# Kernel tuning notes

Measured on AMD Instinct MI355X. Metric: run time of the kernel, lower is better.

The kernel has to match this reference:

```python
import jax, jax.numpy as jnp
import numpy as np

NUM_HEADS = 16
NUM_KV_HEADS = 4
HEAD_SIZE = 128
SCALE = 1.0 / np.sqrt(128.0).astype(np.float32)
NEG_INF = -1e30


def setup_inputs() -> dict:
    key = jax.random.key(0)
    kq, kk, kv = jax.random.split(key, 3)
    B, S = 2, 2048
    query = jax.random.normal(kq, (B, NUM_HEADS, S, HEAD_SIZE), dtype=jnp.float32)
    k = jax.random.normal(kk, (B, NUM_KV_HEADS, S, HEAD_SIZE), dtype=jnp.float32)
    v = jax.random.normal(kv, (B, NUM_KV_HEADS, S, HEAD_SIZE), dtype=jnp.float32)
    return {"query": query, "key": k, "value": v}


def _attn(query, key, value):
    # query: [B, H, S, D]; key/value: [B, Hkv, S, D]; GQA with group = H // Hkv
    B, H, S, D = query.shape
    Hkv = key.shape[1]
    G = H // Hkv
    q = query.reshape(B, Hkv, G, S, D)
    # scores: [B, Hkv, G, Sq, Sk]
    scores = jnp.einsum('bkgsd,bktd->bkgst', q, key) * jnp.float32(SCALE)
    causal = jnp.tril(jnp.ones((S, S), dtype=bool))  # [Sq, Sk]
    scores = jnp.where(causal, scores, jnp.float32(NEG_INF))
    probs = jax.nn.softmax(scores, axis=-1)
    out = jnp.einsum('bkgst,bktd->bkgsd', probs, value)  # [B, Hkv, G, S, D]
    out = out.reshape(B, H, S, D)
    # transpose(1,2).reshape -> [B, S, H*D]
    return out.transpose(0, 2, 1, 3).reshape(B, S, H * D)


def reference(query, key, value):
    return _attn(query, key, value)
```

## Files before the change

kernel.cpp:

```cpp
#include <hip/hip_runtime.h>


#define S_LEN 2048
#define DH    128
#define NH    16
#define NKVH  4
#define NB    2
#define TQ    128
#define TK    64
#define NQT   (S_LEN / TQ)
#define QSCALE 0.12752749610559243f

typedef __attribute__((ext_vector_type(8))) short short8;
typedef __attribute__((ext_vector_type(4))) float f32x4;

#if __has_builtin(__builtin_amdgcn_exp2f)
#define EX2(x) __builtin_amdgcn_exp2f(x)
#else
#define EX2(x) exp2f(x)
#endif

__device__ __forceinline__ unsigned pk2(float a, float b) {
    union { float f; unsigned u; } x, y; x.f = a; y.f = b;
    return ((x.u + 0x8000u) >> 16) | ((y.u + 0x8000u) & 0xffff0000u);
}
__device__ __forceinline__ void cp16(const void* g, void* lds) {
    __builtin_amdgcn_global_load_lds(
        (const __attribute__((address_space(1))) void*)g,
        (__attribute__((address_space(3))) void*)lds, 16, 0, 0);
}

__global__ __launch_bounds__(256, 4)
void prepack(const float* __restrict__ K, const float* __restrict__ V,
             unsigned short* __restrict__ Kb, unsigned short* __restrict__ Vt) {
    if (blockIdx.y == 0) {
        const long long flat = (long long)blockIdx.x * 2048 + threadIdx.x * 8;
        const int s = (int)(flat >> 7) & (S_LEN - 1);
        const int d0 = (int)flat & 127;
        const float* p = K + flat;
        float4 x = *(const float4*)p;
        float4 y = *(const float4*)(p + 4);
        const int cs = (d0 >> 3) ^ (s & 7);
        uint4 o;
        o.x = pk2(x.x, x.y); o.y = pk2(x.z, x.w);
        o.z = pk2(y.x, y.y); o.w = pk2(y.z, y.w);
        *(uint4*)(Kb + (flat & ~127LL) + cs * 8) = o;
    } else {
        const int x = blockIdx.x;
        const int bkvh = x >> 7, sblk = (x >> 2) & 31, q = x & 3;
        const int tid = threadIdx.x;
        __shared__ unsigned Lt[64][17];
        const float* base = V + (size_t)bkvh * S_LEN * DH + (size_t)sblk * 64 * DH + q * 32;
#pragma unroll
        for (int j = 0; j < 2; ++j) {
            const int e = tid + j * 256;
            const int s = e >> 3, c4 = e & 7;
            float4 v = *(const float4*)(base + (size_t)s * DH + c4 * 4);
            Lt[s][c4 * 2]     = pk2(v.x, v.y);
            Lt[s][c4 * 2 + 1] = pk2(v.z, v.w);
        }
        __syncthreads();
        const unsigned short* lt = (const unsigned short*)&Lt[0][0];
        const int d_loc = tid >> 3, pc = tid & 7;
        const int d = q * 32 + d_loc;
        const int c_log = pc ^ (d & 7);
        unsigned short vv[8];
#pragma unroll
        for (int j = 0; j < 8; ++j) {
            const int kp = c_log * 8 + j;
            const int kv = ((kp >> 5) & 1) * 32 + ((kp >> 2) & 1) * 16
                         + ((kp >> 3) & 3) * 4 + (kp & 3);
            vv[j] = lt[kv * 34 + d_loc];
        }
        uint4 o;
        o.x = (unsigned)vv[0] | ((unsigned)vv[1] << 16);
        o.y = (unsigned)vv[2] | ((unsigned)vv[3] << 16);
        o.z = (unsigned)vv[4] | ((unsigned)vv[5] << 16);
        o.w = (unsigned)vv[6] | ((unsigned)vv[7] << 16);
        *(uint4*)(Vt + (size_t)bkvh * S_LEN * DH + (size_t)d * S_LEN + sblk * 64 + pc * 8) = o;
    }
}

__global__ __launch_bounds__(512, 4)
void attn_fwd(const float* __restrict__ Q,
              const unsigned short* __restrict__ Kb,
              const unsigned short* __restrict__ Vtg,
              float* __restrict__ O,
              float* __restrict__ Opart,
              float* __restrict__ Lpart) {
    const int n    = blockIdx.x;
    const int g    = n & 7;
    const int b    = g >> 2;
    const int kvh  = g & 3;
    const int kk   = n >> 3;
    const int h    = kvh * 4 + (kk & 3);
    const int pr   = kk >> 2;
    const int a    = pr & 7;
    const int role = pr >> 3;
    const int sid  = ((b * NH + h) << 3) + a;

    const int tid  = threadIdx.x;
    const int w    = tid >> 6;
    const int lane = tid & 63;
    const int quad = lane >> 4;
    const int l16  = lane & 15;
    const int swz  = l16 & 7;

    int qt0, kt00, nr0, qt1; bool two_seg;
    if (role == 0) { qt0 = a;      kt00 = 0;         nr0 = 2 * a + 2;
                     qt1 = 15 - a; two_seg = true; }
    else           { qt0 = 15 - a; kt00 = 15 - 2*a;  nr0 = 17;
                     qt1 = 0;      two_seg = false; }

    __shared__ alignas(16) unsigned short Kl[2][TK][DH];
    __shared__ alignas(16) unsigned short Vl[2][DH][TK];

    const unsigned short* kb = Kb  + ((size_t)b * NKVH + kvh) * (size_t)(S_LEN * DH);
    const unsigned short* vb = Vtg + ((size_t)b * NKVH + kvh) * (size_t)(S_LEN * DH);

    auto stage = [&](int buf, int kt) {
        const char* ks = (const char*)(kb + (size_t)kt * TK * DH);
        char* kd = (char*)&Kl[buf][0][0];
#pragma unroll
        for (int i = 0; i < 2; ++i) {
            const int off = w * 2048 + i * 1024;
            cp16(ks + off + lane * 16, kd + off);
        }
        const char* vs = (const char*)vb + (size_t)kt * (TK * 2);
        char* vd = (char*)&Vl[buf][0][0];
#pragma unroll
        for (int i = 0; i < 2; ++i) {
            const int off = w * 2048 + i * 1024;
            const int row = w * 16 + i * 8 + (lane >> 3);
            cp16(vs + (size_t)row * (S_LEN * 2) + (lane & 7) * 16, vd + off);
        }
    };
    auto ktof = [&](int r) { return r < nr0 ? kt00 + r : r - nr0; };

    stage(0, ktof(0));

    int qt  = qt0;
    int wq0 = qt * TQ + w * 16;
    int ntw = 2 * qt + 1 + (w >> 2);

    short8 aq[4];
    auto loadQ = [&]() {
        const float* qp = Q + (((size_t)b * NH + h) * S_LEN + wq0 + l16) * DH;
#pragma unroll
        for (int dc = 0; dc < 4; ++dc) {
            float4 xx = *(const float4*)(qp + dc * 32 + quad * 8);
            float4 yy = *(const float4*)(qp + dc * 32 + quad * 8 + 4);
            union { unsigned u[4]; short8 s; } tq;
            tq.u[0] = pk2(xx.x * QSCALE, xx.y * QSCALE);
            tq.u[1] = pk2(xx.z * QSCALE, xx.w * QSCALE);
            tq.u[2] = pk2(yy.x * QSCALE, yy.y * QSCALE);
            tq.u[3] = pk2(yy.z * QSCALE, yy.w * QSCALE);
            aq[dc] = tq.s;
        }
    };
    loadQ();

    f32x4 o[8];
    float lsum = 0.f;
#pragma unroll
    for (int ch = 0; ch < 8; ++ch) o[ch] = (f32x4){0.f, 0.f, 0.f, 0.f};

    __syncthreads();

    int cur = 0;
    for (int r = 0; r < 17; ++r) {
        if (r + 1 < 17) stage(cur ^ 1, ktof(r + 1));
        const int kt = ktof(r);
        if (kt < ntw) {
            const int j0 = kt * TK;
            const bool diag = (kt == ntw - 1);
            f32x4 s[4];
#pragma unroll
            for (int k4 = 0; k4 < 4; ++k4) s[k4] = (f32x4){0.f, 0.f, 0.f, 0.f};
#pragma unroll
            for (int dc = 0; dc < 4; ++dc) {
#pragma unroll
                for (int k4 = 0; k4 < 4; ++k4) {
                    short8 bk = *(const short8*)&Kl[cur][k4 * 16 + l16][((dc * 4 + quad) ^ swz) * 8];
                    s[k4] = __builtin_amdgcn_mfma_f32_16x16x32_bf16(bk, aq[dc], s[k4], 0, 0, 0);
                }
            }
            const int qrow = wq0 + l16;
            float p[4][4];
#pragma unroll
            for (int k4 = 0; k4 < 4; ++k4) {
#pragma unroll
                for (int rr = 0; rr < 4; ++rr) {
                    float v = s[k4][rr];
                    if (diag && (j0 + k4 * 16 + quad * 4 + rr > qrow)) v = -1e30f;
                    const float pe = EX2(v);
                    lsum += pe;
                    p[k4][rr] = pe;
                }
            }
            union { unsigned u[4]; short8 s8; } pa0, pa1;
            pa0.u[0] = pk2(p[0][0], p[0][1]); pa0.u[1] = pk2(p[0][2], p[0][3]);
            pa0.u[2] = pk2(p[1][0], p[1][1]); pa0.u[3] = pk2(p[1][2], p[1][3]);
            pa1.u[0] = pk2(p[2][0], p[2][1]); pa1.u[1] = pk2(p[2][2], p[2][3]);
            pa1.u[2] = pk2(p[3][0], p[3][1]); pa1.u[3] = pk2(p[3][2], p[3][3]);
#pragma unroll
            for (int ch = 0; ch < 8; ++ch) {
                short8 bv0 = *(const short8*)&Vl[cur][ch * 16 + l16][(quad ^ swz) * 8];
                o[ch] = __builtin_amdgcn_mfma_f32_16x16x32_bf16(pa0.s8, bv0, o[ch], 0, 0, 0);
                short8 bv1 = *(const short8*)&Vl[cur][ch * 16 + l16][((4 + quad) ^ swz) * 8];
                o[ch] = __builtin_amdgcn_mfma_f32_16x16x32_bf16(pa1.s8, bv1, o[ch], 0, 0, 0);
            }
        }
        __syncthreads();
        cur ^= 1;
        if (two_seg && r == nr0 - 1) {
            float rs = lsum;
            rs += __shfl_xor(rs, 16);
            rs += __shfl_xor(rs, 32);
#pragma unroll
            for (int rr = 0; rr < 4; ++rr) {
                const float invl = 1.f / __shfl(rs, quad * 4 + rr);
                const int row = wq0 + quad * 4 + rr;
                float* op = O + ((size_t)b * S_LEN + row) * (NH * DH) + h * DH;
#pragma unroll
                for (int ch = 0; ch < 8; ++ch)
                    op[ch * 16 + l16] = o[ch][rr] * invl;
            }
            qt = qt1; wq0 = qt * TQ + w * 16; ntw = 2 * qt + 1 + (w >> 2);
            loadQ();
#pragma unroll
            for (int ch = 0; ch < 8; ++ch) o[ch] = (f32x4){0.f, 0.f, 0.f, 0.f};
            lsum = 0.f;
        }
    }

    float* lb = Lpart + (size_t)(role * 256 + sid) * 128;
    {
        float rs = lsum;
        rs += __shfl_xor(rs, 16);
        rs += __shfl_xor(rs, 32);
        if (lane < 16) lb[w * 16 + l16] = rs;
#pragma unroll
        for (int rr = 0; rr < 4; ++rr) {
            const int rl = w * 16 + quad * 4 + rr;
            float* op;
            if (role == 0) {
                const int row = wq0 + quad * 4 + rr;
                op = O + ((size_t)b * S_LEN + row) * (NH * DH) + h * DH;
            } else {
                op = Opart + (size_t)sid * (128 * 128) + (size_t)rl * 128;
            }
#pragma unroll
            for (int ch = 0; ch < 8; ++ch)
                op[ch * 16 + l16] = o[ch][rr];
        }
    }
}

__global__ __launch_bounds__(256)
void combine(const float* __restrict__ Opart, const float* __restrict__ Lpart,
             float* __restrict__ O) {
    const int blk = blockIdx.x;
    const int sid = blk >> 2;
    const int qp  = blk & 3;
    const int bh = sid >> 3, a = sid & 7;
    const int b = bh >> 4, h = bh & 15;
    const int qt = 15 - a;
    const float* o1 = Opart + (size_t)sid * (128 * 128);
    const float* l0 = Lpart + (size_t)sid * 128;
    const float* l1 = Lpart + (size_t)(256 + sid) * 128;
    const int tid = threadIdx.x;
#pragma unroll
    for (int i = 0; i < 4; ++i) {
        const int idx = qp * 1024 + i * 256 + tid;
        const int row = idx >> 5;
        const int c4  = idx & 31;
        const float inv = 1.f / (l0[row] + l1[row]);
        float* op = O + ((size_t)b * S_LEN + qt * 128 + row) * (NH * DH) + h * DH + c4 * 4;
        const float4 x = *(const float4*)op;
        const float4 y = ((const float4*)o1)[idx];
        float4 z;
        z.x = (x.x + y.x) * inv; z.y = (x.y + y.y) * inv;
        z.z = (x.z + y.z) * inv; z.w = (x.w + y.w) * inv;
        *(float4*)op = z;
    }
}

extern "C" void kernel_launch(void* const* d_in, const int* in_sizes, int n_in,
                              void* d_out, int out_size, void* d_ws, size_t ws_size,
                              hipStream_t stream) {
    const float* Q = (const float*)d_in[0];
    const float* K = (const float*)d_in[1];
    const float* V = (const float*)d_in[2];
    float* O = (float*)d_out;
    unsigned short* Kb = (unsigned short*)d_ws;
    unsigned short* Vt = Kb + (size_t)NB * NKVH * S_LEN * DH;
    float* Opart = (float*)(Vt + (size_t)NB * NKVH * S_LEN * DH);
    float* Lpart = Opart + (size_t)256 * 128 * 128;
    dim3 pgrid(NB * NKVH * (S_LEN / 16), 2);
    prepack<<<pgrid, 256, 0, stream>>>(K, V, Kb, Vt);
    attn_fwd<<<dim3(512), 512, 0, stream>>>(Q, Kb, Vt, O, Opart, Lpart);
    combine<<<dim3(1024), 256, 0, stream>>>(Opart, Lpart, O);
}
```

Baseline: 146.6 us.

## Split KV tile across wave pairs with 32-row query tiles and LDS reduction

Each wave now owns 32 query rows, two 16-row sub-tiles, and half of the 64-key tile. Each K and V fragment read from LDS is reused across two MFMAs, which halves LDS traffic per MFMA. Partial outputs and row sums from paired waves are summed through shared memory, reusing the idle K/V double-buffer slots plus a new 16KB exchange buffer, before the normalize or store step. The cost is more registers for two accumulator sets, extra LDS capacity that may lower occupancy, and several added barriers at segment boundaries.

```diff
diff --git a/kernel.cpp b/kernel.cpp
--- a/kernel.cpp
+++ b/kernel.cpp
@@ -101,6 +101,8 @@
 
     const int tid  = threadIdx.x;
     const int w    = tid >> 6;
+    const int rw   = w >> 1;
+    const int kh   = w & 1;
     const int lane = tid & 63;
     const int quad = lane >> 4;
     const int l16  = lane & 15;
@@ -114,6 +116,7 @@
 
     __shared__ alignas(16) unsigned short Kl[2][TK][DH];
     __shared__ alignas(16) unsigned short Vl[2][DH][TK];
+    __shared__ alignas(16) float XCH[4096];
 
     const unsigned short* kb = Kb  + ((size_t)b * NKVH + kvh) * (size_t)(S_LEN * DH);
     const unsigned short* vb = Vtg + ((size_t)b * NKVH + kvh) * (size_t)(S_LEN * DH);
@@ -139,120 +142,207 @@
 
     stage(0, ktof(0));
 
-    int qt  = qt0;
-    int wq0 = qt * TQ + w * 16;
-    int ntw = 2 * qt + 1 + (w >> 2);
-
-    short8 aq[4];
+    int qt, wq0, ntw;
+    auto setseg = [&](int q) {
+        qt = q; wq0 = qt * TQ + rw * 32;
+        ntw = (wq0 + 31 - kh * 32 + 64) >> 6;
+    };
+    setseg(qt0);
+
+    short8 aq[2][4];
     auto loadQ = [&]() {
-        const float* qp = Q + (((size_t)b * NH + h) * S_LEN + wq0 + l16) * DH;
-#pragma unroll
-        for (int dc = 0; dc < 4; ++dc) {
-            float4 xx = *(const float4*)(qp + dc * 32 + quad * 8);
-            float4 yy = *(const float4*)(qp + dc * 32 + quad * 8 + 4);
-            union { unsigned u[4]; short8 s; } tq;
-            tq.u[0] = pk2(xx.x * QSCALE, xx.y * QSCALE);
-            tq.u[1] = pk2(xx.z * QSCALE, xx.w * QSCALE);
-            tq.u[2] = pk2(yy.x * QSCALE, yy.y * QSCALE);
-            tq.u[3] = pk2(yy.z * QSCALE, yy.w * QSCALE);
-            aq[dc] = tq.s;
+#pragma unroll
+        for (int sub = 0; sub < 2; ++sub) {
+            const float* qp = Q + (((size_t)b * NH + h) * S_LEN + wq0 + sub * 16 + l16) * DH;
+#pragma unroll
+            for (int dc = 0; dc < 4; ++dc) {
+                float4 xx = *(const float4*)(qp + dc * 32 + quad * 8);
+                float4 yy = *(const float4*)(qp + dc * 32 + quad * 8 + 4);
+                union { unsigned u[4]; short8 s; } tq;
+                tq.u[0] = pk2(xx.x * QSCALE, xx.y * QSCALE);
+                tq.u[1] = pk2(xx.z * QSCALE, xx.w * QSCALE);
+                tq.u[2] = pk2(yy.x * QSCALE, yy.y * QSCALE);
+                tq.u[3] = pk2(yy.z * QSCALE, yy.w * QSCALE);
+                aq[sub][dc] = tq.s;
+            }
         }
     };
     loadQ();
 
-    f32x4 o[8];
-    float lsum = 0.f;
-#pragma unroll
-    for (int ch = 0; ch < 8; ++ch) o[ch] = (f32x4){0.f, 0.f, 0.f, 0.f};
+    f32x4 o[2][8];
+    float lsum[2] = {0.f, 0.f};
+#pragma unroll
+    for (int sub = 0; sub < 2; ++sub)
+#pragma unroll
+        for (int ch = 0; ch < 8; ++ch) o[sub][ch] = (f32x4){0.f, 0.f, 0.f, 0.f};
+
+    int cur = 0;
+
+    auto pair_reduce = [&](float rs[2]) {
+        f32x4* dA = (f32x4*)&XCH[0];
+        f32x4* dB = (f32x4*)&Kl[cur ^ 1][0][0];
+        f32x4* dC = (f32x4*)&Vl[cur ^ 1][0][0];
+        float* rsb = (float*)&Kl[cur ^ 1][0][0];
+        if (w == 1 || w == 3 || w == 5) {
+            f32x4* d = (w == 1) ? dA : (w == 3) ? dB : dC;
+#pragma unroll
+            for (int sub = 0; sub < 2; ++sub)
+#pragma unroll
+                for (int ch = 0; ch < 8; ++ch)
+                    d[(sub * 8 + ch) * 64 + lane] = o[sub][ch];
+        }
+        __syncthreads();
+        if (w == 0 || w == 2 || w == 4) {
+            f32x4* d = (w == 0) ? dA : (w == 2) ? dB : dC;
+#pragma unroll
+            for (int sub = 0; sub < 2; ++sub)
+#pragma unroll
+                for (int ch = 0; ch < 8; ++ch)
+                    o[sub][ch] += d[(sub * 8 + ch) * 64 + lane];
+        }
+        __syncthreads();
+        if (w == 7) {
+#pragma unroll
+            for (int sub = 0; sub < 2; ++sub)
+#pragma unroll
+                for (int ch = 0; ch < 8; ++ch)
+                    dA[(sub * 8 + ch) * 64 + lane] = o[sub][ch];
+        }
+        if ((w & 1) && lane < 16) {
+            rsb[rw * 32 + l16]      = rs[0];
+            rsb[rw * 32 + 16 + l16] = rs[1];
+        }
+        __syncthreads();
+        if (w == 6) {
+#pragma unroll
+            for (int sub = 0; sub < 2; ++sub)
+#pragma unroll
+                for (int ch = 0; ch < 8; ++ch)
+                    o[sub][ch] += dA[(sub * 8 + ch) * 64 + lane];
+        }
+        if (!(w & 1)) {
+            rs[0] += rsb[rw * 32 + l16];
+            rs[1] += rsb[rw * 32 + 16 + l16];
+        }
+        __syncthreads();
+    };
+    auto rowsum = [&](float rs[2]) {
+#pragma unroll
+        for (int sub = 0; sub < 2; ++sub) {
+            float t = lsum[sub];
+            t += __shfl_xor(t, 16);
+            t += __shfl_xor(t, 32);
+            rs[sub] = t;
+        }
+    };
 
     __syncthreads();
 
-    int cur = 0;
     for (int r = 0; r < 17; ++r) {
         if (r + 1 < 17) stage(cur ^ 1, ktof(r + 1));
         const int kt = ktof(r);
         if (kt < ntw) {
             const int j0 = kt * TK;
             const bool diag = (kt == ntw - 1);
-            f32x4 s[4];
-#pragma unroll
-            for (int k4 = 0; k4 < 4; ++k4) s[k4] = (f32x4){0.f, 0.f, 0.f, 0.f};
+            f32x4 s[2][2];
+#pragma unroll
+            for (int sub = 0; sub < 2; ++sub)
+#pragma unroll
+                for (int k2 = 0; k2 < 2; ++k2) s[sub][k2] = (f32x4){0.f, 0.f, 0.f, 0.f};
 #pragma unroll
             for (int dc = 0; dc < 4; ++dc) {
 #pragma unroll
-                for (int k4 = 0; k4 < 4; ++k4) {
-                    short8 bk = *(const short8*)&Kl[cur][k4 * 16 + l16][((dc * 4 + quad) ^ swz) * 8];
-                    s[k4] = __builtin_amdgcn_mfma_f32_16x16x32_bf16(bk, aq[dc], s[k4], 0, 0, 0);
+                for (int k2 = 0; k2 < 2; ++k2) {
+                    short8 bk = *(const short8*)&Kl[cur][kh * 32 + k2 * 16 + l16][((dc * 4 + quad) ^ swz) * 8];
+                    s[0][k2] = __builtin_amdgcn_mfma_f32_16x16x32_bf16(bk, aq[0][dc], s[0][k2], 0, 0, 0);
+                    s[1][k2] = __builtin_amdgcn_mfma_f32_16x16x32_bf16(bk, aq[1][dc], s[1][k2], 0, 0, 0);
                 }
             }
-            const int qrow = wq0 + l16;
-            float p[4][4];
-#pragma unroll
-            for (int k4 = 0; k4 < 4; ++k4) {
-#pragma unroll
-                for (int rr = 0; rr < 4; ++rr) {
-                    float v = s[k4][rr];
-                    if (diag && (j0 + k4 * 16 + quad * 4 + rr > qrow)) v = -1e30f;
-                    const float pe = EX2(v);
-                    lsum += pe;
-                    p[k4][rr] = pe;
+            union { unsigned u[4]; short8 s8; } pa[2];
+#pragma unroll
+            for (int sub = 0; sub < 2; ++sub) {
+                const int qrow = wq0 + sub * 16 + l16;
+                float p[2][4];
+#pragma unroll
+                for (int k2 = 0; k2 < 2; ++k2) {
+#pragma unroll
+                    for (int rr = 0; rr < 4; ++rr) {
+                        float v = s[sub][k2][rr];
+                        if (diag && (j0 + kh * 32 + k2 * 16 + quad * 4 + rr > qrow)) v = -1e30f;
+                        const float pe = EX2(v);
+                        lsum[sub] += pe;
+                        p[k2][rr] = pe;
+                    }
                 }
-            }
-            union { unsigned u[4]; short8 s8; } pa0, pa1;
-            pa0.u[0] = pk2(p[0][0], p[0][1]); pa0.u[1] = pk2(p[0][2], p[0][3]);
-            pa0.u[2] = pk2(p[1][0], p[1][1]); pa0.u[3] = pk2(p[1][2], p[1][3]);
-            pa1.u[0] = pk2(p[2][0], p[2][1]); pa1.u[1] = pk2(p[2][2], p[2][3]);
-            pa1.u[2] = pk2(p[3][0], p[3][1]); pa1.u[3] = pk2(p[3][2], p[3][3]);
+                pa[sub].u[0] = pk2(p[0][0], p[0][1]);
+                pa[sub].u[1] = pk2(p[0][2], p[0][3]);
+                pa[sub].u[2] = pk2(p[1][0], p[1][1]);
+                pa[sub].u[3] = pk2(p[1][2], p[1][3]);
+            }
 #pragma unroll
             for (int ch = 0; ch < 8; ++ch) {
-                short8 bv0 = *(const short8*)&Vl[cur][ch * 16 + l16][(quad ^ swz) * 8];
-                o[ch] = __builtin_amdgcn_mfma_f32_16x16x32_bf16(pa0.s8, bv0, o[ch], 0, 0, 0);
-                short8 bv1 = *(const short8*)&Vl[cur][ch * 16 + l16][((4 + quad) ^ swz) * 8];
-                o[ch] = __builtin_amdgcn_mfma_f32_16x16x32_bf16(pa1.s8, bv1, o[ch], 0, 0, 0);
+                short8 bv = *(const short8*)&Vl[cur][ch * 16 + l16][((kh * 4 + quad) ^ swz) * 8];
+                o[0][ch] = __builtin_amdgcn_mfma_f32_16x16x32_bf16(pa[0].s8, bv, o[0][ch], 0, 0, 0);
+                o[1][ch] = __builtin_amdgcn_mfma_f32_16x16x32_bf16(pa[1].s8, bv, o[1][ch], 0, 0, 0);
             }
         }
         __syncthreads();
         cur ^= 1;
         if (two_seg && r == nr0 - 1) {
-            float rs = lsum;
-            rs += __shfl_xor(rs, 16);
-            rs += __shfl_xor(rs, 32);
-#pragma unroll
-            for (int rr = 0; rr < 4; ++rr) {
-                const float invl = 1.f / __shfl(rs, quad * 4 + rr);
-                const int row = wq0 + quad * 4 + rr;
-                float* op = O + ((size_t)b * S_LEN + row) * (NH * DH) + h * DH;
-#pragma unroll
-                for (int ch = 0; ch < 8; ++ch)
-                    op[ch * 16 + l16] = o[ch][rr] * invl;
-            }
-            qt = qt1; wq0 = qt * TQ + w * 16; ntw = 2 * qt + 1 + (w >> 2);
+            float rs[2];
+            rowsum(rs);
+            pair_reduce(rs);
+            if (!(w & 1)) {
+#pragma unroll
+                for (int sub = 0; sub < 2; ++sub) {
+#pragma unroll
+                    for (int rr = 0; rr < 4; ++rr) {
+                        const float invl = 1.f / __shfl(rs[sub], quad * 4 + rr);
+                        const int row = qt0 * TQ + rw * 32 + sub * 16 + quad * 4 + rr;
+                        float* op = O + ((size_t)b * S_LEN + row) * (NH * DH) + h * DH;
+#pragma unroll
+                        for (int ch = 0; ch < 8; ++ch)
+                            op[ch * 16 + l16] = o[sub][ch][rr] * invl;
+                    }
+                }
+            }
+            setseg(qt1);
             loadQ();
 #pragma unroll
-            for (int ch = 0; ch < 8; ++ch) o[ch] = (f32x4){0.f, 0.f, 0.f, 0.f};
-            lsum = 0.f;
+            for (int sub = 0; sub < 2; ++sub)
+#pragma unroll
+                for (int ch = 0; ch < 8; ++ch) o[sub][ch] = (f32x4){0.f, 0.f, 0.f, 0.f};
+            lsum[0] = 0.f; lsum[1] = 0.f;
         }
     }
 
-    float* lb = Lpart + (size_t)(role * 256 + sid) * 128;
     {
-        float rs = lsum;
-        rs += __shfl_xor(rs, 16);
-        rs += __shfl_xor(rs, 32);
-        if (lane < 16) lb[w * 16 + l16] = rs;
-#pragma unroll
-        for (int rr = 0; rr < 4; ++rr) {
-            const int rl = w * 16 + quad * 4 + rr;
-            float* op;
-            if (role == 0) {
-                const int row = wq0 + quad * 4 + rr;
-                op = O + ((size_t)b * S_LEN + row) * (NH * DH) + h * DH;
-            } else {
-                op = Opart + (size_t)sid * (128 * 128) + (size_t)rl * 128;
-            }
-#pragma unroll
-            for (int ch = 0; ch < 8; ++ch)
-                op[ch * 16 + l16] = o[ch][rr];
+        float rs[2];
+        rowsum(rs);
+        pair_reduce(rs);
+        if (!(w & 1)) {
+            float* lb = Lpart + (size_t)(role * 256 + sid) * 128;
+            if (lane < 16) {
+                lb[rw * 32 + l16]      = rs[0];
+                lb[rw * 32 + 16 + l16] = rs[1];
+            }
+#pragma unroll
+            for (int sub = 0; sub < 2; ++sub) {
+#pragma unroll
+                for (int rr = 0; rr < 4; ++rr) {
+                    const int rl = rw * 32 + sub * 16 + quad * 4 + rr;
+                    float* op;
+                    if (role == 0) {
+                        const int row = wq0 + sub * 16 + quad * 4 + rr;
+                        op = O + ((size_t)b * S_LEN + row) * (NH * DH) + h * DH;
+                    } else {
+                        op = Opart + (size_t)sid * (128 * 128) + (size_t)rl * 128;
+                    }
+#pragma unroll
+                    for (int ch = 0; ch < 8; ++ch)
+                        op[ch * 16 + l16] = o[sub][ch][rr];
+                }
+            }
         }
     }
 }
```

Result: slower. 214.3 us (+46.2%).

## Halve query and key tile sizes, doubling workgroups with 4-wave blocks

Applied to the files above, without the earlier changes.

Shrinks the query tile from 128 to 64 rows and the key tile from 64 to 32, runs 1024 workgroups of 256 threads instead of 512 of 512, and reworks the causal pairing schedule, the V transpose/swizzle layout, the stage addressing and the combine indexing to match. The goal is finer load balance and more resident workgroups per CU across the causal triangle. In exchange, each K/V tile is reused by fewer query rows, so global/LDS traffic and sync rounds per FLOP rise.

```diff
diff --git a/kernel.cpp b/kernel.cpp
--- a/kernel.cpp
+++ b/kernel.cpp
@@ -6,9 +6,8 @@
 #define NH    16
 #define NKVH  4
 #define NB    2
-#define TQ    128
-#define TK    64
-#define NQT   (S_LEN / TQ)
+#define TQ    64
+#define TK    32
 #define QSCALE 0.12752749610559243f
 
 typedef __attribute__((ext_vector_type(8))) short short8;
@@ -62,26 +61,26 @@
         __syncthreads();
         const unsigned short* lt = (const unsigned short*)&Lt[0][0];
         const int d_loc = tid >> 3, pc = tid & 7;
+        const int half = pc >> 2, cs = pc & 3;
         const int d = q * 32 + d_loc;
-        const int c_log = pc ^ (d & 7);
+        const int c_log = cs ^ (d & 3);
         unsigned short vv[8];
 #pragma unroll
-        for (int j = 0; j < 8; ++j) {
-            const int kp = c_log * 8 + j;
-            const int kv = ((kp >> 5) & 1) * 32 + ((kp >> 2) & 1) * 16
-                         + ((kp >> 3) & 3) * 4 + (kp & 3);
-            vv[j] = lt[kv * 34 + d_loc];
+        for (int e = 0; e < 8; ++e) {
+            const int kv32 = ((e >> 2) << 4) + c_log * 4 + (e & 3);
+            vv[e] = lt[(half * 32 + kv32) * 34 + d_loc];
         }
         uint4 o;
         o.x = (unsigned)vv[0] | ((unsigned)vv[1] << 16);
         o.y = (unsigned)vv[2] | ((unsigned)vv[3] << 16);
         o.z = (unsigned)vv[4] | ((unsigned)vv[5] << 16);
         o.w = (unsigned)vv[6] | ((unsigned)vv[7] << 16);
-        *(uint4*)(Vt + (size_t)bkvh * S_LEN * DH + (size_t)d * S_LEN + sblk * 64 + pc * 8) = o;
+        *(uint4*)(Vt + (size_t)bkvh * S_LEN * DH + (size_t)d * S_LEN
+                  + sblk * 64 + half * 32 + cs * 8) = o;
     }
 }
 
-__global__ __launch_bounds__(512, 4)
+__global__ __launch_bounds__(256, 4)
 void attn_fwd(const float* __restrict__ Q,
               const unsigned short* __restrict__ Kb,
               const unsigned short* __restrict__ Vtg,
@@ -95,9 +94,9 @@
     const int kk   = n >> 3;
     const int h    = kvh * 4 + (kk & 3);
     const int pr   = kk >> 2;
-    const int a    = pr & 7;
-    const int role = pr >> 3;
-    const int sid  = ((b * NH + h) << 3) + a;
+    const int a    = pr & 15;
+    const int role = pr >> 4;
+    const int sid  = ((b * NH + h) << 4) + a;
 
     const int tid  = threadIdx.x;
     const int w    = tid >> 6;
@@ -107,9 +106,9 @@
     const int swz  = l16 & 7;
 
     int qt0, kt00, nr0, qt1; bool two_seg;
-    if (role == 0) { qt0 = a;      kt00 = 0;         nr0 = 2 * a + 2;
-                     qt1 = 15 - a; two_seg = true; }
-    else           { qt0 = 15 - a; kt00 = 15 - 2*a;  nr0 = 17;
+    if (role == 0) { qt0 = a;      kt00 = 0;          nr0 = 2 * a + 2;
+                     qt1 = 31 - a; two_seg = true; }
+    else           { qt0 = 31 - a; kt00 = 31 - 2 * a; nr0 = 33;
                      qt1 = 0;      two_seg = false; }
 
     __shared__ alignas(16) unsigned short Kl[2][TK][DH];
@@ -123,25 +122,29 @@
         char* kd = (char*)&Kl[buf][0][0];
 #pragma unroll
         for (int i = 0; i < 2; ++i) {
-            const int off = w * 2048 + i * 1024;
-            cp16(ks + off + lane * 16, kd + off);
-        }
-        const char* vs = (const char*)vb + (size_t)kt * (TK * 2);
+            const int off = w * 2048 + i * 1024 + lane * 16;
+            cp16(ks + off, kd + off);
+        }
         char* vd = (char*)&Vl[buf][0][0];
 #pragma unroll
         for (int i = 0; i < 2; ++i) {
-            const int off = w * 2048 + i * 1024;
-            const int row = w * 16 + i * 8 + (lane >> 3);
-            cp16(vs + (size_t)row * (S_LEN * 2) + (lane & 7) * 16, vd + off);
+            const int off = w * 2048 + i * 1024 + lane * 16;
+            const int d = off >> 6;
+            const int c = (lane & 3);
+            cp16((const char*)vb + (size_t)d * (S_LEN * 2) + kt * 64 + c * 16,
+                 vd + off);
         }
     };
     auto ktof = [&](int r) { return r < nr0 ? kt00 + r : r - nr0; };
 
     stage(0, ktof(0));
 
-    int qt  = qt0;
-    int wq0 = qt * TQ + w * 16;
-    int ntw = 2 * qt + 1 + (w >> 2);
+    int qt, wq0, ntw;
+    auto setseg = [&](int q) {
+        qt = q; wq0 = qt * TQ + w * 16;
+        ntw = (wq0 + 47) >> 5;
+    };
+    setseg(qt0);
 
     short8 aq[4];
     auto loadQ = [&]() {
@@ -168,27 +171,27 @@
     __syncthreads();
 
     int cur = 0;
-    for (int r = 0; r < 17; ++r) {
-        if (r + 1 < 17) stage(cur ^ 1, ktof(r + 1));
+    for (int r = 0; r < 33; ++r) {
+        if (r + 1 < 33) stage(cur ^ 1, ktof(r + 1));
         const int kt = ktof(r);
         if (kt < ntw) {
             const int j0 = kt * TK;
             const bool diag = (kt == ntw - 1);
-            f32x4 s[4];
-#pragma unroll
-            for (int k4 = 0; k4 < 4; ++k4) s[k4] = (f32x4){0.f, 0.f, 0.f, 0.f};
+            f32x4 s[2];
+#pragma unroll
+            for (int k4 = 0; k4 < 2; ++k4) s[k4] = (f32x4){0.f, 0.f, 0.f, 0.f};
 #pragma unroll
             for (int dc = 0; dc < 4; ++dc) {
 #pragma unroll
-                for (int k4 = 0; k4 < 4; ++k4) {
+                for (int k4 = 0; k4 < 2; ++k4) {
                     short8 bk = *(const short8*)&Kl[cur][k4 * 16 + l16][((dc * 4 + quad) ^ swz) * 8];
                     s[k4] = __builtin_amdgcn_mfma_f32_16x16x32_bf16(bk, aq[dc], s[k4], 0, 0, 0);
                 }
             }
             const int qrow = wq0 + l16;
-            float p[4][4];
-#pragma unroll
-            for (int k4 = 0; k4 < 4; ++k4) {
+            float p[2][4];
+#pragma unroll
+            for (int k4 = 0; k4 < 2; ++k4) {
 #pragma unroll
                 for (int rr = 0; rr < 4; ++rr) {
                     float v = s[k4][rr];
@@ -198,17 +201,13 @@
                     p[k4][rr] = pe;
                 }
             }
-            union { unsigned u[4]; short8 s8; } pa0, pa1;
-            pa0.u[0] = pk2(p[0][0], p[0][1]); pa0.u[1] = pk2(p[0][2], p[0][3]);
-            pa0.u[2] = pk2(p[1][0], p[1][1]); pa0.u[3] = pk2(p[1][2], p[1][3]);
-            pa1.u[0] = pk2(p[2][0], p[2][1]); pa1.u[1] = pk2(p[2][2], p[2][3]);
-            pa1.u[2] = pk2(p[3][0], p[3][1]); pa1.u[3] = pk2(p[3][2], p[3][3]);
+            union { unsigned u[4]; short8 s8; } pa;
+            pa.u[0] = pk2(p[0][0], p[0][1]); pa.u[1] = pk2(p[0][2], p[0][3]);
+            pa.u[2] = pk2(p[1][0], p[1][1]); pa.u[3] = pk2(p[1][2], p[1][3]);
 #pragma unroll
             for (int ch = 0; ch < 8; ++ch) {
-                short8 bv0 = *(const short8*)&Vl[cur][ch * 16 + l16][(quad ^ swz) * 8];
-                o[ch] = __builtin_amdgcn_mfma_f32_16x16x32_bf16(pa0.s8, bv0, o[ch], 0, 0, 0);
-                short8 bv1 = *(const short8*)&Vl[cur][ch * 16 + l16][((4 + quad) ^ swz) * 8];
-                o[ch] = __builtin_amdgcn_mfma_f32_16x16x32_bf16(pa1.s8, bv1, o[ch], 0, 0, 0);
+                short8 bv = *(const short8*)&Vl[cur][ch * 16 + l16][(quad ^ (l16 & 3)) * 8];
+                o[ch] = __builtin_amdgcn_mfma_f32_16x16x32_bf16(pa.s8, bv, o[ch], 0, 0, 0);
             }
         }
         __syncthreads();
@@ -226,7 +225,7 @@
                 for (int ch = 0; ch < 8; ++ch)
                     op[ch * 16 + l16] = o[ch][rr] * invl;
             }
-            qt = qt1; wq0 = qt * TQ + w * 16; ntw = 2 * qt + 1 + (w >> 2);
+            setseg(qt1);
             loadQ();
 #pragma unroll
             for (int ch = 0; ch < 8; ++ch) o[ch] = (f32x4){0.f, 0.f, 0.f, 0.f};
@@ -234,8 +233,8 @@
         }
     }
 
-    float* lb = Lpart + (size_t)(role * 256 + sid) * 128;
     {
+        float* lb = Lpart + (size_t)(role * 512 + sid) * 64;
         float rs = lsum;
         rs += __shfl_xor(rs, 16);
         rs += __shfl_xor(rs, 32);
@@ -248,7 +247,7 @@
                 const int row = wq0 + quad * 4 + rr;
                 op = O + ((size_t)b * S_LEN + row) * (NH * DH) + h * DH;
             } else {
-                op = Opart + (size_t)sid * (128 * 128) + (size_t)rl * 128;
+                op = Opart + (size_t)sid * (64 * 128) + (size_t)rl * 128;
             }
 #pragma unroll
             for (int ch = 0; ch < 8; ++ch)
@@ -260,23 +259,23 @@
 __global__ __launch_bounds__(256)
 void combine(const float* __restrict__ Opart, const float* __restrict__ Lpart,
              float* __restrict__ O) {
-    const int blk = blockIdx.x;
-    const int sid = blk >> 2;
-    const int qp  = blk & 3;
-    const int bh = sid >> 3, a = sid & 7;
+    const int blk  = blockIdx.x;
+    const int sid  = blk >> 1;
+    const int half = blk & 1;
+    const int bh = sid >> 4, a = sid & 15;
     const int b = bh >> 4, h = bh & 15;
-    const int qt = 15 - a;
-    const float* o1 = Opart + (size_t)sid * (128 * 128);
-    const float* l0 = Lpart + (size_t)sid * 128;
-    const float* l1 = Lpart + (size_t)(256 + sid) * 128;
+    const int qt = 31 - a;
+    const float* o1 = Opart + (size_t)sid * (64 * 128);
+    const float* l0 = Lpart + (size_t)sid * 64;
+    const float* l1 = Lpart + (size_t)(512 + sid) * 64;
     const int tid = threadIdx.x;
 #pragma unroll
     for (int i = 0; i < 4; ++i) {
-        const int idx = qp * 1024 + i * 256 + tid;
+        const int idx = half * 1024 + i * 256 + tid;
         const int row = idx >> 5;
         const int c4  = idx & 31;
         const float inv = 1.f / (l0[row] + l1[row]);
-        float* op = O + ((size_t)b * S_LEN + qt * 128 + row) * (NH * DH) + h * DH + c4 * 4;
+        float* op = O + ((size_t)b * S_LEN + qt * 64 + row) * (NH * DH) + h * DH + c4 * 4;
         const float4 x = *(const float4*)op;
         const float4 y = ((const float4*)o1)[idx];
         float4 z;
@@ -296,9 +295,9 @@
     unsigned short* Kb = (unsigned short*)d_ws;
     unsigned short* Vt = Kb + (size_t)NB * NKVH * S_LEN * DH;
     float* Opart = (float*)(Vt + (size_t)NB * NKVH * S_LEN * DH);
-    float* Lpart = Opart + (size_t)256 * 128 * 128;
+    float* Lpart = Opart + (size_t)512 * 64 * 128;
     dim3 pgrid(NB * NKVH * (S_LEN / 16), 2);
     prepack<<<pgrid, 256, 0, stream>>>(K, V, Kb, Vt);
-    attn_fwd<<<dim3(512), 512, 0, stream>>>(Q, Kb, Vt, O, Opart, Lpart);
+    attn_fwd<<<dim3(1024), 256, 0, stream>>>(Q, Kb, Vt, O, Opart, Lpart);
     combine<<<dim3(1024), 256, 0, stream>>>(Opart, Lpart, O);
 }
```

Result: slower. 150.3 us (+2.6%).
